# Optimization experiments

Hardware: AMD Instinct MI355X
Metric: run time of the kernel (lower is better)

The kernel has to match this reference:

```python
import jax, jax.numpy as jnp
import numpy as np

N_NODES = 50000
N_EDGES = 1600000
N_GRAPHS = 512
IN_DIM = 64
HID = 128
OUT_DIM = 10


def setup_inputs() -> dict:
    key = jax.random.key(0)
    ks = jax.random.split(key, 12)
    x = jax.random.normal(ks[0], (N_NODES, IN_DIM), dtype=jnp.float32)
    edge_index = jax.random.randint(ks[1], (2, N_EDGES), 0, N_NODES, dtype=jnp.int64)
    batch = jnp.sort(jax.random.randint(ks[2], (N_NODES,), 0, N_GRAPHS, dtype=jnp.int64))
    edge_attr = jax.random.uniform(ks[3], (N_EDGES,), dtype=jnp.float32)
    # glorot-ish init for weights
    def lin(k, fan_in, fan_out):
        s = (6.0 / (fan_in + fan_out)) ** 0.5
        return jax.random.uniform(k, (fan_in, fan_out), minval=-s, maxval=s, dtype=jnp.float32)
    return {
        "x": x, "edge_index": edge_index, "batch": batch, "edge_attr": edge_attr,
        "W1": lin(ks[4], IN_DIM, HID), "b1": jnp.zeros((HID,), jnp.float32),
        "W2": lin(ks[5], HID, HID), "b2": jnp.zeros((HID,), jnp.float32),
        "Wm1": lin(ks[6], HID, HID), "bm1": jnp.zeros((HID,), jnp.float32),
        "Wm2": lin(ks[7], HID, OUT_DIM), "bm2": jnp.zeros((OUT_DIM,), jnp.float32),
    }


def _gcn_conv(x, edge_index, edge_weight, W, b, num_nodes):
    """PyG GCNConv: add self-loops, symmetric norm with edge weights, x@W, scatter-add, +bias."""
    loop = jnp.arange(num_nodes, dtype=edge_index.dtype)
    src = jnp.concatenate([edge_index[0], loop])
    dst = jnp.concatenate([edge_index[1], loop])
    ew = jnp.concatenate([edge_weight, jnp.ones((num_nodes,), edge_weight.dtype)])
    deg = jax.ops.segment_sum(ew, dst, num_segments=num_nodes)  # [N]
    dinv = jnp.where(deg > 0, jax.lax.rsqrt(jnp.where(deg > 0, deg, 1.0)), 0.0)
    norm = dinv[src] * ew * dinv[dst]  # [E+N]
    h = x @ W  # [N, F_out]
    msg = h[src] * norm[:, None]  # gather + scale
    out = jax.ops.segment_sum(msg, dst, num_segments=num_nodes)
    return out + b


def reference(x, edge_index, batch, edge_attr, W1, b1, W2, b2, Wm1, bm1, Wm2, bm2):
    n = x.shape[0]
    h = _gcn_conv(x, edge_index, edge_attr, W1, b1, n)
    h = jax.nn.relu(h)  # dropout = identity in eval mode
    h = _gcn_conv(h, edge_index, edge_attr, W2, b2, n)
    h = jax.nn.relu(h)
    pooled = jax.ops.segment_sum(h, batch, num_segments=N_GRAPHS)  # global_add_pool
    z = jax.nn.relu(pooled @ Wm1 + bm1)
    return z @ Wm2 + bm2  # [num_graphs, out_dim]
```

## Files before the change

kernel.cpp:

```cpp
#include <hip/hip_runtime.h>
#include <hip/hip_bf16.h>
#include <hip/hip_fp16.h>
#include <cstdint>

#define HIDC 128
#define FIXSCALE 4194304.0f
#define FIXINV   (1.0f / 4194304.0f)
#define MAXDEG 80

#define BKT_SHIFT 7
#define BKT_NODES 128
#define BKT_CAP   4608
#define BIN_TILE  4096
#define BIN_THREADS 512

typedef _Float16 half8 __attribute__((ext_vector_type(8)));
typedef float float4v __attribute__((ext_vector_type(4)));

__global__ __launch_bounds__(256) void prep_kernel(
        const float* __restrict__ W1, const float* __restrict__ W2,
        _Float16* __restrict__ W1t, _Float16* __restrict__ W2t,
        unsigned int* __restrict__ tails, int nbkt) {
    int i = blockIdx.x * 256 + threadIdx.x;
    if (i < 16384) { int k = i >> 7, n = i & 127; W2t[n * 128 + k] = (_Float16)W2[i]; }
    if (i < 8192)  { int k = i >> 7, n = i & 127; W1t[n * 64 + k]  = (_Float16)W1[i]; }
    if (i < nbkt) tails[i] = 0u;
}

__global__ __launch_bounds__(BIN_THREADS) void bin_kernel(
        const int* __restrict__ ei, const float* __restrict__ ea,
        unsigned int* __restrict__ buck_lo, unsigned char* __restrict__ buck_dl,
        unsigned int* __restrict__ tails, int E, int nbkt) {
    __shared__ unsigned long long rec[BIN_TILE];
    __shared__ unsigned int cnt[BIN_THREADS];
    __shared__ unsigned int startx[BIN_THREADS];
    __shared__ unsigned int cur[BIN_THREADS];
    __shared__ unsigned int gbase[BIN_THREADS];
    __shared__ unsigned int wtot[BIN_THREADS / 64];
    int t = threadIdx.x;
    int base = blockIdx.x * BIN_TILE;
    int total = E - base; if (total > BIN_TILE) total = BIN_TILE;

    cnt[t] = 0;
    __syncthreads();

    unsigned int lo[8], dv[8];
#pragma unroll
    for (int j = 0; j < 8; ++j) {
        int e = base + j * BIN_THREADS + t;
        if (e < E) {
            int s = ei[e]; int d = ei[E + e]; float w = ea[e];
            lo[j] = (unsigned int)s |
                    ((unsigned int)__half_as_ushort(__float2half_rn(w)) << 16);
            dv[j] = (unsigned int)d;
            atomicAdd(&cnt[dv[j] >> BKT_SHIFT], 1u);
        } else dv[j] = 0xffffffffu;
    }
    __syncthreads();

    unsigned int c = cnt[t];
    unsigned int sc = c;
#pragma unroll
    for (int off = 1; off < 64; off <<= 1) {
        unsigned int v = __shfl_up(sc, off);
        if ((t & 63) >= off) sc += v;
    }
    if ((t & 63) == 63) wtot[t >> 6] = sc;
    __syncthreads();
    unsigned int wbase = 0;
    int w = t >> 6;
    for (int i = 0; i < w; ++i) wbase += wtot[i];
    unsigned int excl = sc + wbase - c;
    startx[t] = excl;
    cur[t] = excl;
    if (t < nbkt) gbase[t] = atomicAdd(&tails[t], c);
    __syncthreads();

#pragma unroll
    for (int j = 0; j < 8; ++j) {
        if (dv[j] != 0xffffffffu) {
            unsigned int p = atomicAdd(&cur[dv[j] >> BKT_SHIFT], 1u);
            rec[p] = ((unsigned long long)dv[j] << 32) | (unsigned long long)lo[j];
        }
    }
    __syncthreads();

    for (int i = t; i < total; i += BIN_THREADS) {
        unsigned long long r = rec[i];
        unsigned int hi = (unsigned int)(r >> 32);
        unsigned int b = hi >> BKT_SHIFT;
        unsigned int idx = gbase[b] + ((unsigned int)i - startx[b]);
        if (idx < BKT_CAP) {
            buck_lo[b * BKT_CAP + idx] = (unsigned int)r;
            buck_dl[b * BKT_CAP + idx] = (unsigned char)(hi & (BKT_NODES - 1));
        }
    }
}

__global__ __launch_bounds__(256) void fill_kernel(
        const unsigned int* __restrict__ buck_lo,
        const unsigned char* __restrict__ buck_dl,
        const unsigned int* __restrict__ tails,
        const float* __restrict__ x,
        unsigned long long* __restrict__ degcnt,
        unsigned int* __restrict__ padcsr,
        _Float16* __restrict__ xt, int n_nodes) {
    __shared__ unsigned long long deg[BKT_NODES];
    __shared__ float sdinv[BKT_NODES];
    int b = blockIdx.x, t = threadIdx.x;
    if (t < BKT_NODES) deg[t] = 0ull;
    __syncthreads();
    int cnt_b = (int)tails[b]; if (cnt_b > BKT_CAP) cnt_b = BKT_CAP;
    unsigned int boff = (unsigned int)b * BKT_CAP;
    int nodeBase = b << BKT_SHIFT;
    for (int i = t; i < cnt_b; i += 256) {
        unsigned int lo = buck_lo[boff + i];
        unsigned int dl = buck_dl[boff + i];
        float w = __half2float(__ushort_as_half((unsigned short)(lo >> 16)));
        unsigned int fx = (unsigned int)(w * FIXSCALE + 0.5f);
        unsigned long long old =
            atomicAdd(&deg[dl], (1ull << 32) | (unsigned long long)fx);
        unsigned int rank = (unsigned int)(old >> 32);
        if (rank < MAXDEG)
            padcsr[(size_t)(nodeBase + dl) * MAXDEG + rank] = lo;
    }
    __syncthreads();
    if (t < BKT_NODES) {
        unsigned long long dv = deg[t];
        sdinv[t] = rsqrtf(1.0f + (float)(unsigned int)(dv & 0xffffffffull) * FIXINV);
        int node = nodeBase + t;
        if (node < n_nodes) degcnt[node] = dv;
    }
    __syncthreads();
    int d = t & 63, nl = t >> 6;
    for (int nn = nl; nn < BKT_NODES; nn += 4) {
        int node = nodeBase + nn;
        if (node < n_nodes)
            xt[(size_t)node * 64 + d] = (_Float16)(x[(size_t)node * 64 + d] * sdinv[nn]);
    }
}

__global__ __launch_bounds__(256) void agg0_kernel(
        const _Float16* __restrict__ xt,
        const unsigned long long* __restrict__ degcnt,
        const unsigned int* __restrict__ padcsr,
        _Float16* __restrict__ g, int n_nodes) {
    int wave = threadIdx.x >> 6, lane = threadIdx.x & 63;
    int node = blockIdx.x * 4 + wave;
    if (node >= n_nodes) return;
    int half = lane >> 5, li = lane & 31;
    unsigned long long v = degcnt[node];
    int cnt = (int)(v >> 32); if (cnt > MAXDEG) cnt = MAXDEG;
    float di = rsqrtf(1.0f + (float)(unsigned int)(v & 0xffffffffull) * FIXINV);
    const unsigned int* row = padcsr + (size_t)node * MAXDEG;
    const __half2* X = (const __half2*)xt;
    float a0 = 0.f, a1 = 0.f;
    int e = 0;
    for (; e + 32 <= cnt; e += 32) {
        unsigned int p[16];
#pragma unroll
        for (int j = 0; j < 16; ++j) p[j] = row[e + 2 * j + half];
        __half2 vv[16];
#pragma unroll
        for (int j = 0; j < 16; ++j)
            vv[j] = X[(p[j] & 0xffffu) * 32u + (unsigned)li];
#pragma unroll
        for (int j = 0; j < 16; ++j) {
            __half ch = __ushort_as_half((unsigned short)(p[j] >> 16));
            a0 = fmaf(__half2float(ch), __half2float(__low2half(vv[j])), a0);
            a1 = fmaf(__half2float(ch), __half2float(__high2half(vv[j])), a1);
        }
    }
    if (e < cnt) {
        int rem = cnt - e;
        unsigned int p[16]; bool m[16];
#pragma unroll
        for (int j = 0; j < 16; ++j) {
            int idx = 2 * j + half;
            m[j] = idx < rem;
            p[j] = m[j] ? row[e + idx] : 0u;
        }
        __half2 vv[16];
#pragma unroll
        for (int j = 0; j < 16; ++j)
            vv[j] = X[(p[j] & 0xffffu) * 32u + (unsigned)li];
#pragma unroll
        for (int j = 0; j < 16; ++j) {
            __half ch = m[j] ? __ushort_as_half((unsigned short)(p[j] >> 16))
                             : __ushort_as_half((unsigned short)0);
            a0 = fmaf(__half2float(ch), __half2float(__low2half(vv[j])), a0);
            a1 = fmaf(__half2float(ch), __half2float(__high2half(vv[j])), a1);
        }
    }
    if (half == 0) {
        float2 f = __half22float2(X[(unsigned)node * 32u + (unsigned)li]);
        a0 += f.x; a1 += f.y;
    }
    a0 += __shfl_xor(a0, 32);
    a1 += __shfl_xor(a1, 32);
    if (half == 0)
        *((__half2*)g + (unsigned)node * 32u + li) = __floats2half2_rn(di * a0, di * a1);
}

__global__ __launch_bounds__(256) void agg2_kernel(const __half* __restrict__ h,
                                                   const unsigned long long* __restrict__ degcnt,
                                                   const unsigned int* __restrict__ padcsr,
                                                   __half* __restrict__ out, int n_nodes) {
    int wave = threadIdx.x >> 6;
    int lane = threadIdx.x & 63;
    int node = blockIdx.x * 4 + wave;
    if (node >= n_nodes) return;
    int half = lane >> 5, li = lane & 31;
    unsigned long long v = degcnt[node];
    int cnt = (int)(v >> 32);
    if (cnt > MAXDEG) cnt = MAXDEG;
    float di = rsqrtf(1.0f + (float)(unsigned int)(v & 0xffffffffull) * FIXINV);
    const unsigned int* row = padcsr + (size_t)node * MAXDEG;
    float a0 = 0.f, a1 = 0.f, a2 = 0.f, a3 = 0.f;
    int e = 0;
    for (; e + 32 <= cnt; e += 32) {
        unsigned int p[16];
#pragma unroll
        for (int j = 0; j < 16; ++j) p[j] = row[e + 2 * j + half];
        float2 vv[16];
#pragma unroll
        for (int j = 0; j < 16; ++j)
            vv[j] = *reinterpret_cast<const float2*>(
                h + (p[j] & 0xffffu) * (unsigned)HIDC + (unsigned)(li * 4));
#pragma unroll
        for (int j = 0; j < 16; ++j) {
            __half ch = __ushort_as_half((unsigned short)(p[j] >> 16));
            __half2 h01 = *reinterpret_cast<const __half2*>(&vv[j].x);
            __half2 h23 = *reinterpret_cast<const __half2*>(&vv[j].y);
            a0 = fmaf(__half2float(ch), __half2float(__low2half(h01)), a0);
            a1 = fmaf(__half2float(ch), __half2float(__high2half(h01)), a1);
            a2 = fmaf(__half2float(ch), __half2float(__low2half(h23)), a2);
            a3 = fmaf(__half2float(ch), __half2float(__high2half(h23)), a3);
        }
    }
    if (e < cnt) {
        int rem = cnt - e;
        unsigned int p[16]; bool m[16];
#pragma unroll
        for (int j = 0; j < 16; ++j) {
            int idx = 2 * j + half;
            m[j] = idx < rem;
            p[j] = m[j] ? row[e + idx] : 0u;
        }
        float2 vv[16];
#pragma unroll
        for (int j = 0; j < 16; ++j)
            vv[j] = *reinterpret_cast<const float2*>(
                h + (p[j] & 0xffffu) * (unsigned)HIDC + (unsigned)(li * 4));
#pragma unroll
        for (int j = 0; j < 16; ++j) {
            __half ch = m[j] ? __ushort_as_half((unsigned short)(p[j] >> 16))
                             : __ushort_as_half((unsigned short)0);
            __half2 h01 = *reinterpret_cast<const __half2*>(&vv[j].x);
            __half2 h23 = *reinterpret_cast<const __half2*>(&vv[j].y);
            a0 = fmaf(__half2float(ch), __half2float(__low2half(h01)), a0);
            a1 = fmaf(__half2float(ch), __half2float(__high2half(h01)), a1);
            a2 = fmaf(__half2float(ch), __half2float(__low2half(h23)), a2);
            a3 = fmaf(__half2float(ch), __half2float(__high2half(h23)), a3);
        }
    }
    if (half == 0) {
        float2 w = *reinterpret_cast<const float2*>(
            h + (unsigned)node * (unsigned)HIDC + (unsigned)(li * 4));
        __half2 h01 = *reinterpret_cast<const __half2*>(&w.x);
        __half2 h23 = *reinterpret_cast<const __half2*>(&w.y);
        a0 += __half2float(__low2half(h01));
        a1 += __half2float(__high2half(h01));
        a2 += __half2float(__low2half(h23));
        a3 += __half2float(__high2half(h23));
    }
    a0 += __shfl_xor(a0, 32);
    a1 += __shfl_xor(a1, 32);
    a2 += __shfl_xor(a2, 32);
    a3 += __shfl_xor(a3, 32);
    if (half == 0) {
        __half2 o01 = __floats2half2_rn(di * a0, di * a1);
        __half2 o23 = __floats2half2_rn(di * a2, di * a3);
        uint2 st;
        st.x = *reinterpret_cast<unsigned int*>(&o01);
        st.y = *reinterpret_cast<unsigned int*>(&o23);
        *reinterpret_cast<uint2*>(out + (size_t)node * HIDC + li * 4) = st;
    }
}

__global__ __launch_bounds__(256) void gemm1_mfma_kernel(
        const _Float16* __restrict__ G,
        const _Float16* __restrict__ W1t,
        const float* __restrict__ b1,
        const unsigned long long* __restrict__ degcnt,
        __half* __restrict__ out, int n_nodes) {
    int wave = threadIdx.x >> 6, lane = threadIdx.x & 63;
    int nodeBase = (blockIdx.x * 4 + wave) * 16;
    if (nodeBase >= n_nodes) return;
    int mrow = lane & 15, quad = lane >> 4;

    int anode = nodeBase + mrow; if (anode >= n_nodes) anode = n_nodes - 1;
    const _Float16* Arow = G + (size_t)anode * 64 + quad * 8;
    half8 a[2];
    a[0] = *(const half8*)(Arow);
    a[1] = *(const half8*)(Arow + 32);

    float4v acc[8];
#pragma unroll
    for (int nt = 0; nt < 8; ++nt) acc[nt] = (float4v)(0.f);
#pragma unroll
    for (int nt = 0; nt < 8; ++nt) {
        const _Float16* Brow = W1t + (size_t)(nt * 16 + mrow) * 64 + quad * 8;
#pragma unroll
        for (int q = 0; q < 2; ++q) {
            half8 b = *(const half8*)(Brow + q * 32);
            acc[nt] = __builtin_amdgcn_mfma_f32_16x16x32_f16(a[q], b, acc[nt], 0, 0, 0);
        }
    }
#pragma unroll
    for (int r = 0; r < 4; ++r) {
        int node = nodeBase + quad * 4 + r;
        if (node < n_nodes) {
            unsigned long long v = degcnt[node];
            float di = rsqrtf(1.0f + (float)(unsigned int)(v & 0xffffffffull) * FIXINV);
#pragma unroll
            for (int nt = 0; nt < 8; ++nt) {
                int col = nt * 16 + mrow;
                float val = fmaxf(acc[nt][r] + b1[col], 0.f) * di;
                out[(size_t)node * 128 + col] = __float2half(val);
            }
        }
    }
}

__global__ __launch_bounds__(256) void gemm2_mfma_kernel(
        const __half* __restrict__ A,
        const _Float16* __restrict__ W2t,
        const float* __restrict__ b2,
        __half* __restrict__ out, int n_nodes) {
    int wave = threadIdx.x >> 6, lane = threadIdx.x & 63;
    int nodeBase = (blockIdx.x * 4 + wave) * 16;
    if (nodeBase >= n_nodes) return;
    int mrow = lane & 15, quad = lane >> 4;

    int anode = nodeBase + mrow; if (anode >= n_nodes) anode = n_nodes - 1;
    const _Float16* Arow = (const _Float16*)A + (size_t)anode * 128 + quad * 8;
    half8 a[4];
#pragma unroll
    for (int q = 0; q < 4; ++q) a[q] = *(const half8*)(Arow + q * 32);

    float4v acc[8];
#pragma unroll
    for (int nt = 0; nt < 8; ++nt) acc[nt] = (float4v)(0.f);
#pragma unroll
    for (int nt = 0; nt < 8; ++nt) {
        const _Float16* Brow = W2t + (size_t)(nt * 16 + mrow) * 128 + quad * 8;
#pragma unroll
        for (int q = 0; q < 4; ++q) {
            half8 b = *(const half8*)(Brow + q * 32);
            acc[nt] = __builtin_amdgcn_mfma_f32_16x16x32_f16(a[q], b, acc[nt], 0, 0, 0);
        }
    }
#pragma unroll
    for (int r = 0; r < 4; ++r) {
        int node = nodeBase + quad * 4 + r;
        if (node < n_nodes) {
#pragma unroll
            for (int nt = 0; nt < 8; ++nt) {
                int col = nt * 16 + mrow;
                float val = fmaxf(acc[nt][r] + b2[col], 0.f);
                out[(size_t)node * 128 + col] = __float2half(val);
            }
        }
    }
}

__global__ __launch_bounds__(256) void pool_mlp_kernel(const __half* __restrict__ h,
                                                       const int* __restrict__ batch,
                                                       const float* __restrict__ Wm1,
                                                       const float* __restrict__ bm1,
                                                       const float* __restrict__ Wm2,
                                                       const float* __restrict__ bm2,
                                                       float* __restrict__ out,
                                                       int n_nodes, int out_dim) {
    int g = blockIdx.x;
    int t = threadIdx.x;
    __shared__ int sb[2];
    __shared__ float row2[256];
    __shared__ float row[128];
    __shared__ float zl[128];
    if (t < 2) {
        int target = g + t;
        int lo = 0, hi = n_nodes;
        while (lo < hi) { int mid = (lo + hi) >> 1; if (batch[mid] < target) lo = mid + 1; else hi = mid; }
        sb[t] = lo;
    }
    __syncthreads();
    int beg = sb[0], end = sb[1];
    int dim = t & 127, sub = t >> 7;
    float p = 0.f;
    for (int i = beg + sub; i < end; i += 2)
        p += __half2float(h[(size_t)i * 128 + dim]);
    row2[t] = p;
    __syncthreads();
    if (t < 128) row[t] = row2[t] + row2[t + 128];
    __syncthreads();
    if (t < 128) {
        float acc = bm1[t];
#pragma unroll 8
        for (int k = 0; k < 128; ++k) acc += row[k] * Wm1[k * 128 + t];
        zl[t] = fmaxf(acc, 0.f);
    }
    __syncthreads();
    if (t < out_dim) {
        float o = bm2[t];
#pragma unroll 8
        for (int k = 0; k < 128; ++k) o += zl[k] * Wm2[k * out_dim + t];
        out[g * out_dim + t] = o;
    }
}

extern "C" void kernel_launch(void* const* d_in, const int* in_sizes, int n_in,
                              void* d_out, int out_size, void* d_ws, size_t ws_size,
                              hipStream_t stream) {
    const float* x   = (const float*)d_in[0];
    const int*   ei  = (const int*)d_in[1];
    const int*   bat = (const int*)d_in[2];
    const float* ea  = (const float*)d_in[3];
    const float* W1  = (const float*)d_in[4];
    const float* b1  = (const float*)d_in[5];
    const float* W2  = (const float*)d_in[6];
    const float* b2  = (const float*)d_in[7];
    const float* Wm1 = (const float*)d_in[8];
    const float* bm1 = (const float*)d_in[9];
    const float* Wm2 = (const float*)d_in[10];
    const float* bm2 = (const float*)d_in[11];
    float* out = (float*)d_out;

    const int N = in_sizes[2];
    const int E = in_sizes[1] / 2;
    const int N_GRAPHS = 512;
    const int OUT_DIM = out_size / N_GRAPHS;

    char* ws = (char*)d_ws;
    size_t off = 0;
    auto alloc = [&](size_t bytes) { char* p = ws + off; off += (bytes + 255) & ~size_t(255); return p; };
    char* regB = alloc((size_t)N * HIDC * 2);
    char* regC = alloc((size_t)N * HIDC * 2);
    char* regA = alloc((size_t)N * MAXDEG * 4);
    unsigned long long* degcnt = (unsigned long long*)alloc((size_t)N * 8);
    _Float16* W2t = (_Float16*)alloc(128 * 128 * 2);
    _Float16* W1t = (_Float16*)alloc(128 * 64 * 2);
    unsigned int* tails = (unsigned int*)alloc(BIN_THREADS * 4);

    int nbkt = (N + BKT_NODES - 1) >> BKT_SHIFT;
    unsigned int*  buck_lo = (unsigned int*)regB;
    unsigned char* buck_dl = (unsigned char*)(regB + (size_t)nbkt * BKT_CAP * 4);
    __half*    htld = (__half*)regB;
    _Float16*  xt   = (_Float16*)regC;
    _Float16*  gbuf = (_Float16*)(regC + (size_t)N * 64 * 2);
    __half*    ubuf = (__half*)regC;
    unsigned int* padcsr = (unsigned int*)regA;
    __half*    zbuf = (__half*)regA;

    prep_kernel<<<64, 256, 0, stream>>>(W1, W2, W1t, W2t, tails, nbkt);
    int binBlocks = (E + BIN_TILE - 1) / BIN_TILE;
    bin_kernel<<<binBlocks, BIN_THREADS, 0, stream>>>(ei, ea, buck_lo, buck_dl, tails, E, nbkt);
    fill_kernel<<<nbkt, 256, 0, stream>>>(buck_lo, buck_dl, tails, x, degcnt, padcsr, xt, N);
    agg0_kernel<<<(N + 3) / 4, 256, 0, stream>>>(xt, degcnt, padcsr, gbuf, N);
    gemm1_mfma_kernel<<<(N + 63) / 64, 256, 0, stream>>>(gbuf, W1t, b1, degcnt, htld, N);
    agg2_kernel<<<(N + 3) / 4, 256, 0, stream>>>(htld, degcnt, padcsr, ubuf, N);
    gemm2_mfma_kernel<<<(N + 63) / 64, 256, 0, stream>>>(ubuf, W2t, b2, zbuf, N);
    pool_mlp_kernel<<<N_GRAPHS, 256, 0, stream>>>(zbuf, bat, Wm1, bm1, Wm2, bm2, out, N, OUT_DIM);
}
```

Baseline: 271.4 us.

## Fuse neighbor aggregation with MFMA GEMM per 16-node tile via LDS

Merges each aggregation kernel with the following MFMA GEMM: a block of 4 waves aggregates 16 nodes into shared memory, then each wave computes two 16-column output tiles from LDS. This removes the intermediate global write and read of the aggregated features and two kernel launches. It also zero-pads each CSR row to a multiple of 8 in fill_kernel so the tail loop runs unmasked in chunks of 8. In exchange, each wave now processes 4 nodes serially, the tail is handled in smaller chunks with less memory-level parallelism, and zbuf moves to a different buffer region.

```diff
diff --git a/kernel.cpp b/kernel.cpp
--- a/kernel.cpp
+++ b/kernel.cpp
@@ -129,7 +129,13 @@
         unsigned long long dv = deg[t];
         sdinv[t] = rsqrtf(1.0f + (float)(unsigned int)(dv & 0xffffffffull) * FIXINV);
         int node = nodeBase + t;
-        if (node < n_nodes) degcnt[node] = dv;
+        if (node < n_nodes) {
+            degcnt[node] = dv;
+            int cw = (int)(dv >> 32); if (cw > MAXDEG) cw = MAXDEG;
+            int cp = (cw + 7) & ~7;
+            for (int r = cw; r < cp; ++r)
+                padcsr[(size_t)node * MAXDEG + r] = 0u;
+        }
     }
     __syncthreads();
     int d = t & 63, nl = t >> 6;
@@ -140,235 +146,213 @@
     }
 }
 
-__global__ __launch_bounds__(256) void agg0_kernel(
+__global__ __launch_bounds__(256) void agg0_gemm1_kernel(
         const _Float16* __restrict__ xt,
         const unsigned long long* __restrict__ degcnt,
         const unsigned int* __restrict__ padcsr,
-        _Float16* __restrict__ g, int n_nodes) {
-    int wave = threadIdx.x >> 6, lane = threadIdx.x & 63;
-    int node = blockIdx.x * 4 + wave;
-    if (node >= n_nodes) return;
-    int half = lane >> 5, li = lane & 31;
-    unsigned long long v = degcnt[node];
-    int cnt = (int)(v >> 32); if (cnt > MAXDEG) cnt = MAXDEG;
-    float di = rsqrtf(1.0f + (float)(unsigned int)(v & 0xffffffffull) * FIXINV);
-    const unsigned int* row = padcsr + (size_t)node * MAXDEG;
-    const __half2* X = (const __half2*)xt;
-    float a0 = 0.f, a1 = 0.f;
-    int e = 0;
-    for (; e + 32 <= cnt; e += 32) {
-        unsigned int p[16];
-#pragma unroll
-        for (int j = 0; j < 16; ++j) p[j] = row[e + 2 * j + half];
-        __half2 vv[16];
-#pragma unroll
-        for (int j = 0; j < 16; ++j)
-            vv[j] = X[(p[j] & 0xffffu) * 32u + (unsigned)li];
-#pragma unroll
-        for (int j = 0; j < 16; ++j) {
-            __half ch = __ushort_as_half((unsigned short)(p[j] >> 16));
-            a0 = fmaf(__half2float(ch), __half2float(__low2half(vv[j])), a0);
-            a1 = fmaf(__half2float(ch), __half2float(__high2half(vv[j])), a1);
-        }
-    }
-    if (e < cnt) {
-        int rem = cnt - e;
-        unsigned int p[16]; bool m[16];
-#pragma unroll
-        for (int j = 0; j < 16; ++j) {
-            int idx = 2 * j + half;
-            m[j] = idx < rem;
-            p[j] = m[j] ? row[e + idx] : 0u;
-        }
-        __half2 vv[16];
-#pragma unroll
-        for (int j = 0; j < 16; ++j)
-            vv[j] = X[(p[j] & 0xffffu) * 32u + (unsigned)li];
-#pragma unroll
-        for (int j = 0; j < 16; ++j) {
-            __half ch = m[j] ? __ushort_as_half((unsigned short)(p[j] >> 16))
-                             : __ushort_as_half((unsigned short)0);
-            a0 = fmaf(__half2float(ch), __half2float(__low2half(vv[j])), a0);
-            a1 = fmaf(__half2float(ch), __half2float(__high2half(vv[j])), a1);
-        }
-    }
-    if (half == 0) {
-        float2 f = __half22float2(X[(unsigned)node * 32u + (unsigned)li]);
-        a0 += f.x; a1 += f.y;
-    }
-    a0 += __shfl_xor(a0, 32);
-    a1 += __shfl_xor(a1, 32);
-    if (half == 0)
-        *((__half2*)g + (unsigned)node * 32u + li) = __floats2half2_rn(di * a0, di * a1);
-}
-
-__global__ __launch_bounds__(256) void agg2_kernel(const __half* __restrict__ h,
-                                                   const unsigned long long* __restrict__ degcnt,
-                                                   const unsigned int* __restrict__ padcsr,
-                                                   __half* __restrict__ out, int n_nodes) {
-    int wave = threadIdx.x >> 6;
-    int lane = threadIdx.x & 63;
-    int node = blockIdx.x * 4 + wave;
-    if (node >= n_nodes) return;
-    int half = lane >> 5, li = lane & 31;
-    unsigned long long v = degcnt[node];
-    int cnt = (int)(v >> 32);
-    if (cnt > MAXDEG) cnt = MAXDEG;
-    float di = rsqrtf(1.0f + (float)(unsigned int)(v & 0xffffffffull) * FIXINV);
-    const unsigned int* row = padcsr + (size_t)node * MAXDEG;
-    float a0 = 0.f, a1 = 0.f, a2 = 0.f, a3 = 0.f;
-    int e = 0;
-    for (; e + 32 <= cnt; e += 32) {
-        unsigned int p[16];
-#pragma unroll
-        for (int j = 0; j < 16; ++j) p[j] = row[e + 2 * j + half];
-        float2 vv[16];
-#pragma unroll
-        for (int j = 0; j < 16; ++j)
-            vv[j] = *reinterpret_cast<const float2*>(
-                h + (p[j] & 0xffffu) * (unsigned)HIDC + (unsigned)(li * 4));
-#pragma unroll
-        for (int j = 0; j < 16; ++j) {
-            __half ch = __ushort_as_half((unsigned short)(p[j] >> 16));
-            __half2 h01 = *reinterpret_cast<const __half2*>(&vv[j].x);
-            __half2 h23 = *reinterpret_cast<const __half2*>(&vv[j].y);
-            a0 = fmaf(__half2float(ch), __half2float(__low2half(h01)), a0);
-            a1 = fmaf(__half2float(ch), __half2float(__high2half(h01)), a1);
-            a2 = fmaf(__half2float(ch), __half2float(__low2half(h23)), a2);
-            a3 = fmaf(__half2float(ch), __half2float(__high2half(h23)), a3);
-        }
-    }
-    if (e < cnt) {
-        int rem = cnt - e;
-        unsigned int p[16]; bool m[16];
-#pragma unroll
-        for (int j = 0; j < 16; ++j) {
-            int idx = 2 * j + half;
-            m[j] = idx < rem;
-            p[j] = m[j] ? row[e + idx] : 0u;
-        }
-        float2 vv[16];
-#pragma unroll
-        for (int j = 0; j < 16; ++j)
-            vv[j] = *reinterpret_cast<const float2*>(
-                h + (p[j] & 0xffffu) * (unsigned)HIDC + (unsigned)(li * 4));
-#pragma unroll
-        for (int j = 0; j < 16; ++j) {
-            __half ch = m[j] ? __ushort_as_half((unsigned short)(p[j] >> 16))
-                             : __ushort_as_half((unsigned short)0);
-            __half2 h01 = *reinterpret_cast<const __half2*>(&vv[j].x);
-            __half2 h23 = *reinterpret_cast<const __half2*>(&vv[j].y);
-            a0 = fmaf(__half2float(ch), __half2float(__low2half(h01)), a0);
-            a1 = fmaf(__half2float(ch), __half2float(__high2half(h01)), a1);
-            a2 = fmaf(__half2float(ch), __half2float(__low2half(h23)), a2);
-            a3 = fmaf(__half2float(ch), __half2float(__high2half(h23)), a3);
-        }
-    }
-    if (half == 0) {
-        float2 w = *reinterpret_cast<const float2*>(
-            h + (unsigned)node * (unsigned)HIDC + (unsigned)(li * 4));
-        __half2 h01 = *reinterpret_cast<const __half2*>(&w.x);
-        __half2 h23 = *reinterpret_cast<const __half2*>(&w.y);
-        a0 += __half2float(__low2half(h01));
-        a1 += __half2float(__high2half(h01));
-        a2 += __half2float(__low2half(h23));
-        a3 += __half2float(__high2half(h23));
-    }
-    a0 += __shfl_xor(a0, 32);
-    a1 += __shfl_xor(a1, 32);
-    a2 += __shfl_xor(a2, 32);
-    a3 += __shfl_xor(a3, 32);
-    if (half == 0) {
-        __half2 o01 = __floats2half2_rn(di * a0, di * a1);
-        __half2 o23 = __floats2half2_rn(di * a2, di * a3);
-        uint2 st;
-        st.x = *reinterpret_cast<unsigned int*>(&o01);
-        st.y = *reinterpret_cast<unsigned int*>(&o23);
-        *reinterpret_cast<uint2*>(out + (size_t)node * HIDC + li * 4) = st;
-    }
-}
-
-__global__ __launch_bounds__(256) void gemm1_mfma_kernel(
-        const _Float16* __restrict__ G,
         const _Float16* __restrict__ W1t,
         const float* __restrict__ b1,
+        __half* __restrict__ out, int n_nodes) {
+    __shared__ _Float16 gl[16][72];
+    __shared__ float sdi[16];
+    int wave = threadIdx.x >> 6, lane = threadIdx.x & 63;
+    int tileBase = blockIdx.x * 16;
+    int half = lane >> 5, li = lane & 31;
+    const __half2* X = (const __half2*)xt;
+
+    for (int i = 0; i < 4; ++i) {
+        int nl = wave * 4 + i;
+        int node = tileBase + nl;
+        if (node >= n_nodes) continue;
+        unsigned long long v = degcnt[node];
+        int cnt = (int)(v >> 32); if (cnt > MAXDEG) cnt = MAXDEG;
+        int cntp = (cnt + 7) & ~7;
+        float di = rsqrtf(1.0f + (float)(unsigned int)(v & 0xffffffffull) * FIXINV);
+        const unsigned int* row = padcsr + (size_t)node * MAXDEG;
+        float a0 = 0.f, a1 = 0.f;
+        int e = 0;
+        for (; e + 32 <= cntp; e += 32) {
+            unsigned int p[16];
+#pragma unroll
+            for (int j = 0; j < 16; ++j) p[j] = row[e + 2 * j + half];
+            __half2 vv[16];
+#pragma unroll
+            for (int j = 0; j < 16; ++j)
+                vv[j] = X[(p[j] & 0xffffu) * 32u + (unsigned)li];
+#pragma unroll
+            for (int j = 0; j < 16; ++j) {
+                __half ch = __ushort_as_half((unsigned short)(p[j] >> 16));
+                a0 = fmaf(__half2float(ch), __half2float(__low2half(vv[j])), a0);
+                a1 = fmaf(__half2float(ch), __half2float(__high2half(vv[j])), a1);
+            }
+        }
+        while (e < cntp) {
+            unsigned int p[4];
+#pragma unroll
+            for (int j = 0; j < 4; ++j) p[j] = row[e + 2 * j + half];
+            __half2 vv[4];
+#pragma unroll
+            for (int j = 0; j < 4; ++j)
+                vv[j] = X[(p[j] & 0xffffu) * 32u + (unsigned)li];
+#pragma unroll
+            for (int j = 0; j < 4; ++j) {
+                __half ch = __ushort_as_half((unsigned short)(p[j] >> 16));
+                a0 = fmaf(__half2float(ch), __half2float(__low2half(vv[j])), a0);
+                a1 = fmaf(__half2float(ch), __half2float(__high2half(vv[j])), a1);
+            }
+            e += 8;
+        }
+        if (half == 0) {
+            float2 f = __half22float2(X[(unsigned)node * 32u + (unsigned)li]);
+            a0 += f.x; a1 += f.y;
+        }
+        a0 += __shfl_xor(a0, 32);
+        a1 += __shfl_xor(a1, 32);
+        if (half == 0) {
+            *reinterpret_cast<__half2*>(&gl[nl][li * 2]) =
+                __floats2half2_rn(di * a0, di * a1);
+            if (li == 0) sdi[nl] = di;
+        }
+    }
+    __syncthreads();
+
+    int mrow = lane & 15, quad = lane >> 4;
+    half8 a[2];
+    a[0] = *(const half8*)&gl[mrow][quad * 8];
+    a[1] = *(const half8*)&gl[mrow][quad * 8 + 32];
+#pragma unroll
+    for (int s = 0; s < 2; ++s) {
+        int nt = wave * 2 + s;
+        float4v acc = (float4v)(0.f);
+        const _Float16* Brow = W1t + (size_t)(nt * 16 + mrow) * 64 + quad * 8;
+        half8 b0 = *(const half8*)(Brow);
+        half8 b1v = *(const half8*)(Brow + 32);
+        acc = __builtin_amdgcn_mfma_f32_16x16x32_f16(a[0], b0, acc, 0, 0, 0);
+        acc = __builtin_amdgcn_mfma_f32_16x16x32_f16(a[1], b1v, acc, 0, 0, 0);
+        int col = nt * 16 + mrow;
+        float bb = b1[col];
+#pragma unroll
+        for (int r = 0; r < 4; ++r) {
+            int node = tileBase + quad * 4 + r;
+            if (node < n_nodes) {
+                float val = fmaxf(acc[r] + bb, 0.f) * sdi[quad * 4 + r];
+                out[(size_t)node * 128 + col] = __float2half(val);
+            }
+        }
+    }
+}
+
+__global__ __launch_bounds__(256) void agg2_gemm2_kernel(
+        const __half* __restrict__ h,
         const unsigned long long* __restrict__ degcnt,
-        __half* __restrict__ out, int n_nodes) {
-    int wave = threadIdx.x >> 6, lane = threadIdx.x & 63;
-    int nodeBase = (blockIdx.x * 4 + wave) * 16;
-    if (nodeBase >= n_nodes) return;
-    int mrow = lane & 15, quad = lane >> 4;
-
-    int anode = nodeBase + mrow; if (anode >= n_nodes) anode = n_nodes - 1;
-    const _Float16* Arow = G + (size_t)anode * 64 + quad * 8;
-    half8 a[2];
-    a[0] = *(const half8*)(Arow);
-    a[1] = *(const half8*)(Arow + 32);
-
-    float4v acc[8];
-#pragma unroll
-    for (int nt = 0; nt < 8; ++nt) acc[nt] = (float4v)(0.f);
-#pragma unroll
-    for (int nt = 0; nt < 8; ++nt) {
-        const _Float16* Brow = W1t + (size_t)(nt * 16 + mrow) * 64 + quad * 8;
-#pragma unroll
-        for (int q = 0; q < 2; ++q) {
-            half8 b = *(const half8*)(Brow + q * 32);
-            acc[nt] = __builtin_amdgcn_mfma_f32_16x16x32_f16(a[q], b, acc[nt], 0, 0, 0);
-        }
-    }
-#pragma unroll
-    for (int r = 0; r < 4; ++r) {
-        int node = nodeBase + quad * 4 + r;
-        if (node < n_nodes) {
-            unsigned long long v = degcnt[node];
-            float di = rsqrtf(1.0f + (float)(unsigned int)(v & 0xffffffffull) * FIXINV);
-#pragma unroll
-            for (int nt = 0; nt < 8; ++nt) {
-                int col = nt * 16 + mrow;
-                float val = fmaxf(acc[nt][r] + b1[col], 0.f) * di;
-                out[(size_t)node * 128 + col] = __float2half(val);
-            }
-        }
-    }
-}
-
-__global__ __launch_bounds__(256) void gemm2_mfma_kernel(
-        const __half* __restrict__ A,
+        const unsigned int* __restrict__ padcsr,
         const _Float16* __restrict__ W2t,
         const float* __restrict__ b2,
         __half* __restrict__ out, int n_nodes) {
+    __shared__ __half ul[16][136];
     int wave = threadIdx.x >> 6, lane = threadIdx.x & 63;
-    int nodeBase = (blockIdx.x * 4 + wave) * 16;
-    if (nodeBase >= n_nodes) return;
+    int tileBase = blockIdx.x * 16;
+    int half = lane >> 5, li = lane & 31;
+
+    for (int i = 0; i < 4; ++i) {
+        int nl = wave * 4 + i;
+        int node = tileBase + nl;
+        if (node >= n_nodes) continue;
+        unsigned long long v = degcnt[node];
+        int cnt = (int)(v >> 32); if (cnt > MAXDEG) cnt = MAXDEG;
+        int cntp = (cnt + 7) & ~7;
+        float di = rsqrtf(1.0f + (float)(unsigned int)(v & 0xffffffffull) * FIXINV);
+        const unsigned int* row = padcsr + (size_t)node * MAXDEG;
+        float a0 = 0.f, a1 = 0.f, a2 = 0.f, a3 = 0.f;
+        int e = 0;
+        for (; e + 32 <= cntp; e += 32) {
+            unsigned int p[16];
+#pragma unroll
+            for (int j = 0; j < 16; ++j) p[j] = row[e + 2 * j + half];
+            float2 vv[16];
+#pragma unroll
+            for (int j = 0; j < 16; ++j)
+                vv[j] = *reinterpret_cast<const float2*>(
+                    h + (p[j] & 0xffffu) * (unsigned)HIDC + (unsigned)(li * 4));
+#pragma unroll
+            for (int j = 0; j < 16; ++j) {
+                __half ch = __ushort_as_half((unsigned short)(p[j] >> 16));
+                __half2 h01 = *reinterpret_cast<const __half2*>(&vv[j].x);
+                __half2 h23 = *reinterpret_cast<const __half2*>(&vv[j].y);
+                a0 = fmaf(__half2float(ch), __half2float(__low2half(h01)), a0);
+                a1 = fmaf(__half2float(ch), __half2float(__high2half(h01)), a1);
+                a2 = fmaf(__half2float(ch), __half2float(__low2half(h23)), a2);
+                a3 = fmaf(__half2float(ch), __half2float(__high2half(h23)), a3);
+            }
+        }
+        while (e < cntp) {
+            unsigned int p[4];
+#pragma unroll
+            for (int j = 0; j < 4; ++j) p[j] = row[e + 2 * j + half];
+            float2 vv[4];
+#pragma unroll
+            for (int j = 0; j < 4; ++j)
+                vv[j] = *reinterpret_cast<const float2*>(
+                    h + (p[j] & 0xffffu) * (unsigned)HIDC + (unsigned)(li * 4));
+#pragma unroll
+            for (int j = 0; j < 4; ++j) {
+                __half ch = __ushort_as_half((unsigned short)(p[j] >> 16));
+                __half2 h01 = *reinterpret_cast<const __half2*>(&vv[j].x);
+                __half2 h23 = *reinterpret_cast<const __half2*>(&vv[j].y);
+                a0 = fmaf(__half2float(ch), __half2float(__low2half(h01)), a0);
+                a1 = fmaf(__half2float(ch), __half2float(__high2half(h01)), a1);
+                a2 = fmaf(__half2float(ch), __half2float(__low2half(h23)), a2);
+                a3 = fmaf(__half2float(ch), __half2float(__high2half(h23)), a3);
+            }
+            e += 8;
+        }
+        if (half == 0) {
+            float2 w = *reinterpret_cast<const float2*>(
+                h + (unsigned)node * (unsigned)HIDC + (unsigned)(li * 4));
+            __half2 h01 = *reinterpret_cast<const __half2*>(&w.x);
+            __half2 h23 = *reinterpret_cast<const __half2*>(&w.y);
+            a0 += __half2float(__low2half(h01));
+            a1 += __half2float(__high2half(h01));
+            a2 += __half2float(__low2half(h23));
+            a3 += __half2float(__high2half(h23));
+        }
+        a0 += __shfl_xor(a0, 32);
+        a1 += __shfl_xor(a1, 32);
+        a2 += __shfl_xor(a2, 32);
+        a3 += __shfl_xor(a3, 32);
+        if (half == 0) {
+            __half2 o01 = __floats2half2_rn(di * a0, di * a1);
+            __half2 o23 = __floats2half2_rn(di * a2, di * a3);
+            uint2 st;
+            st.x = *reinterpret_cast<unsigned int*>(&o01);
+            st.y = *reinterpret_cast<unsigned int*>(&o23);
+            *reinterpret_cast<uint2*>(&ul[nl][li * 4]) = st;
+        }
+    }
+    __syncthreads();
+
     int mrow = lane & 15, quad = lane >> 4;
-
-    int anode = nodeBase + mrow; if (anode >= n_nodes) anode = n_nodes - 1;
-    const _Float16* Arow = (const _Float16*)A + (size_t)anode * 128 + quad * 8;
     half8 a[4];
 #pragma unroll
-    for (int q = 0; q < 4; ++q) a[q] = *(const half8*)(Arow + q * 32);
-
-    float4v acc[8];
-#pragma unroll
-    for (int nt = 0; nt < 8; ++nt) acc[nt] = (float4v)(0.f);
-#pragma unroll
-    for (int nt = 0; nt < 8; ++nt) {
+    for (int q = 0; q < 4; ++q)
+        a[q] = *(const half8*)&ul[mrow][quad * 8 + q * 32];
+#pragma unroll
+    for (int s = 0; s < 2; ++s) {
+        int nt = wave * 2 + s;
+        float4v acc = (float4v)(0.f);
         const _Float16* Brow = W2t + (size_t)(nt * 16 + mrow) * 128 + quad * 8;
 #pragma unroll
         for (int q = 0; q < 4; ++q) {
             half8 b = *(const half8*)(Brow + q * 32);
-            acc[nt] = __builtin_amdgcn_mfma_f32_16x16x32_f16(a[q], b, acc[nt], 0, 0, 0);
-        }
-    }
-#pragma unroll
-    for (int r = 0; r < 4; ++r) {
-        int node = nodeBase + quad * 4 + r;
-        if (node < n_nodes) {
-#pragma unroll
-            for (int nt = 0; nt < 8; ++nt) {
-                int col = nt * 16 + mrow;
-                float val = fmaxf(acc[nt][r] + b2[col], 0.f);
+            acc = __builtin_amdgcn_mfma_f32_16x16x32_f16(a[q], b, acc, 0, 0, 0);
+        }
+        int col = nt * 16 + mrow;
+        float bb = b2[col];
+#pragma unroll
+        for (int r = 0; r < 4; ++r) {
+            int node = tileBase + quad * 4 + r;
+            if (node < n_nodes) {
+                float val = fmaxf(acc[r] + bb, 0.f);
                 out[(size_t)node * 128 + col] = __float2half(val);
             }
         }
@@ -458,18 +442,14 @@
     unsigned char* buck_dl = (unsigned char*)(regB + (size_t)nbkt * BKT_CAP * 4);
     __half*    htld = (__half*)regB;
     _Float16*  xt   = (_Float16*)regC;
-    _Float16*  gbuf = (_Float16*)(regC + (size_t)N * 64 * 2);
-    __half*    ubuf = (__half*)regC;
+    __half*    zbuf = (__half*)regC;
     unsigned int* padcsr = (unsigned int*)regA;
-    __half*    zbuf = (__half*)regA;
 
     prep_kernel<<<64, 256, 0, stream>>>(W1, W2, W1t, W2t, tails, nbkt);
     int binBlocks = (E + BIN_TILE - 1) / BIN_TILE;
     bin_kernel<<<binBlocks, BIN_THREADS, 0, stream>>>(ei, ea, buck_lo, buck_dl, tails, E, nbkt);
     fill_kernel<<<nbkt, 256, 0, stream>>>(buck_lo, buck_dl, tails, x, degcnt, padcsr, xt, N);
-    agg0_kernel<<<(N + 3) / 4, 256, 0, stream>>>(xt, degcnt, padcsr, gbuf, N);
-    gemm1_mfma_kernel<<<(N + 63) / 64, 256, 0, stream>>>(gbuf, W1t, b1, degcnt, htld, N);
-    agg2_kernel<<<(N + 3) / 4, 256, 0, stream>>>(htld, degcnt, padcsr, ubuf, N);
-    gemm2_mfma_kernel<<<(N + 63) / 64, 256, 0, stream>>>(ubuf, W2t, b2, zbuf, N);
+    agg0_gemm1_kernel<<<(N + 15) / 16, 256, 0, stream>>>(xt, degcnt, padcsr, W1t, b1, htld, N);
+    agg2_gemm2_kernel<<<(N + 15) / 16, 256, 0, stream>>>(htld, degcnt, padcsr, W2t, b2, zbuf, N);
     pool_mlp_kernel<<<N_GRAPHS, 256, 0, stream>>>(zbuf, bat, Wm1, bm1, Wm2, bm2, out, N, OUT_DIM);
 }
```

Result: no change. 272.9 us (+0.6%).
